# Kernel optimization log

Measured on AMD Instinct MI355X. Metric: run time of the kernel, lower is better.

The kernel has to match this reference:

```python
import jax, jax.numpy as jnp
import numpy as np

EMBED = 256
HEADS = 8
N_EDGES = 32  # topk k per query node = head_edges * heads = number_of_edges
HEAD_DIM = EMBED // HEADS


def setup_inputs() -> dict:
    key = jax.random.key(0)
    k1, k2, k3, k4 = jax.random.split(key, 4)
    B, L = 8, 2048
    return {
        "keys": jax.random.normal(k1, (B, L, EMBED), dtype=jnp.float32),
        "query": jax.random.normal(k2, (B, L, EMBED), dtype=jnp.float32),
        "Wk": jax.random.normal(k3, (HEAD_DIM, HEAD_DIM), dtype=jnp.float32) / np.sqrt(HEAD_DIM).astype(np.float32),
        "Wq": jax.random.normal(k4, (HEAD_DIM, HEAD_DIM), dtype=jnp.float32) / np.sqrt(HEAD_DIM).astype(np.float32),
    }


def reference(keys, query, Wk, Wq):
    B, Lk, _ = keys.shape
    Lq = query.shape[1]
    # split heads: [B, L, H, D]
    k = keys.reshape(B, Lk, HEADS, HEAD_DIM)
    q = query.reshape(B, Lq, HEADS, HEAD_DIM)
    # per-head linear projections (torch Linear: y = x @ W^T, no bias)
    k = jnp.einsum('nkhd,ed->nkhe', k, Wk)
    q = jnp.einsum('nqhd,ed->nqhe', q, Wq)
    # attention scores [B, H, Lq, Lk]
    energy = jnp.einsum('nqhd,nkhd->nhqk', q, k)
    attn = jax.nn.softmax(energy / jnp.sqrt(jnp.float32(EMBED)), axis=3)
    # mean over heads -> [B, Lq, Lk]
    mean_attn = jnp.mean(attn, axis=1)
    # topk neighbor indices per query node, then sorted ascending
    _, idx = jax.lax.top_k(mean_attn, N_EDGES)          # [B, Lq, N_EDGES]
    edges = jnp.sort(idx, axis=2)
    nodes = jnp.broadcast_to(jnp.arange(Lq, dtype=edges.dtype)[None, :, None], edges.shape)
    # edge_index [B, 2, Lq * N_EDGES]: row0 = source node, row1 = neighbor
    edge_index = jnp.stack([nodes.reshape(B, -1), edges.reshape(B, -1)], axis=1)
    return edge_index
```

## Files before the change

kernel.cpp:

```cpp
#include <hip/hip_runtime.h>
#include <hip/hip_bf16.h>

#define NB 8
#define LSEQ 2048
#define HH 8
#define DD 32
#define EE 256
#define NE 32
#define QT 16
#define NWAVE 16
#define NTH 1024
#define KW 128
#define NTILE 8
#define SMS 2050

typedef __attribute__((ext_vector_type(8))) short short8;
typedef __attribute__((ext_vector_type(4))) float f32x4;

__global__ __launch_bounds__(256) void proj_kernel(const float* __restrict__ x,
                                                   const float* __restrict__ W,
                                                   float scale,
                                                   __hip_bfloat16* __restrict__ o1,
                                                   __hip_bfloat16* __restrict__ o2,
                                                   __hip_bfloat16* __restrict__ o3) {
  const int b = blockIdx.x;
  __shared__ float xs[EE];
  __shared__ float Ws[DD][DD + 1];
  const int t = threadIdx.x;
  xs[t] = x[(size_t)b * EE + t];
  for (int i = t; i < DD * DD; i += 256) Ws[i / DD][i % DD] = W[i];
  __syncthreads();
  const int h = t / DD, e = t % DD;
  float acc = 0.f;
#pragma unroll
  for (int d = 0; d < DD; ++d) acc = fmaf(xs[h * DD + d], Ws[e][d], acc);
  acc *= scale;
  const int n = b / LSEQ, l = b % LSEQ;
  const size_t oi = (((size_t)n * HH + h) * LSEQ + l) * DD + e;
  __hip_bfloat16 p1 = __float2bfloat16(acc);
  float r1 = acc - __bfloat162float(p1);
  __hip_bfloat16 p2 = __float2bfloat16(r1);
  float r2 = r1 - __bfloat162float(p2);
  __hip_bfloat16 p3 = __float2bfloat16(r2);
  o1[oi] = p1;
  o2[oi] = p2;
  o3[oi] = p3;
}

__global__ __launch_bounds__(NTH) void attn_topk_kernel(
    const __hip_bfloat16* __restrict__ q1, const __hip_bfloat16* __restrict__ q2,
    const __hip_bfloat16* __restrict__ q3, const __hip_bfloat16* __restrict__ k1,
    const __hip_bfloat16* __restrict__ k2, const __hip_bfloat16* __restrict__ k3,
    int* __restrict__ out) {
  __shared__ float smean[QT * SMS];
  __shared__ float wredS[2][QT][NWAVE];

  const int t = threadIdx.x;
  const int w = t >> 6, l = t & 63;
  const int g = l >> 4, c = l & 15;
  const int n = blockIdx.x & 7;
  const int q0 = (blockIdx.x >> 3) * QT;

  for (int i = t; i < QT * SMS; i += NTH) smean[i] = 0.f;
  float* macc = &smean[(g * 4) * SMS + w * KW + c];
  __syncthreads();

  for (int h = 0; h < HH; ++h) {
    const size_t hb = ((size_t)n * HH + h) * LSEQ;
    const size_t qoff = (hb + q0 + c) * DD + (size_t)g * 8;
    const short8 aH = *(const short8*)(q1 + qoff);
    const short8 aM = *(const short8*)(q2 + qoff);
    const short8 aL = *(const short8*)(q3 + qoff);

    f32x4 acc[NTILE];
#pragma unroll
    for (int t2 = 0; t2 < NTILE; ++t2) {
      const size_t koff = (hb + (size_t)w * KW + t2 * 16 + c) * DD + (size_t)g * 8;
      const short8 bH = *(const short8*)(k1 + koff);
      const short8 bM = *(const short8*)(k2 + koff);
      const short8 bL = *(const short8*)(k3 + koff);
      f32x4 a = {0.f, 0.f, 0.f, 0.f};
      a = __builtin_amdgcn_mfma_f32_16x16x32_bf16(aH, bH, a, 0, 0, 0);
      a = __builtin_amdgcn_mfma_f32_16x16x32_bf16(aH, bM, a, 0, 0, 0);
      a = __builtin_amdgcn_mfma_f32_16x16x32_bf16(aM, bH, a, 0, 0, 0);
      a = __builtin_amdgcn_mfma_f32_16x16x32_bf16(aH, bL, a, 0, 0, 0);
      a = __builtin_amdgcn_mfma_f32_16x16x32_bf16(aL, bH, a, 0, 0, 0);
      a = __builtin_amdgcn_mfma_f32_16x16x32_bf16(aM, bM, a, 0, 0, 0);
      acc[t2] = a;
    }

    float Zl[4] = {0.f, 0.f, 0.f, 0.f};
#pragma unroll
    for (int t2 = 0; t2 < NTILE; ++t2) {
#pragma unroll
      for (int r = 0; r < 4; ++r) {
        float e = exp2f(acc[t2][r]);
        acc[t2][r] = e;
        Zl[r] += e;
      }
    }
#pragma unroll
    for (int msk = 1; msk <= 8; msk <<= 1)
#pragma unroll
      for (int r = 0; r < 4; ++r) Zl[r] += __shfl_xor(Zl[r], msk);
    if (c == 0) {
#pragma unroll
      for (int r = 0; r < 4; ++r) wredS[h & 1][g * 4 + r][w] = Zl[r];
    }
    __syncthreads();
    float inv[4];
#pragma unroll
    for (int r = 0; r < 4; ++r) {
      float z = wredS[h & 1][g * 4 + r][c];
#pragma unroll
      for (int msk = 1; msk <= 8; msk <<= 1) z += __shfl_xor(z, msk);
      inv[r] = __builtin_amdgcn_rcpf(z);
    }
#pragma unroll
    for (int t2 = 0; t2 < NTILE; ++t2)
#pragma unroll
      for (int r = 0; r < 4; ++r) {
        float* p = macc + r * SMS + t2 * 16;
        *p = fmaf(acc[t2][r], inv[r], *p);
      }
  }
  __syncthreads();

  float* row = &smean[w * SMS];
  float vals[32];
  float v1 = -1e30f, v2 = -1e30f;
  int i1 = 1 << 30, i2 = 1 << 30;
#pragma unroll
  for (int j = 0; j < 32; ++j) {
    float v = row[j * 64 + l];
    vals[j] = v;
    const int k = j * 64 + l;
    if (v > v1) { v2 = v1; i2 = i1; v1 = v; i1 = k; }
    else if (v > v2) { v2 = v; i2 = k; }
  }
  unsigned rem = 0u;
  int selk = 0;
#pragma unroll 1
  for (int it = 0; it < NE; ++it) {
    float bv = v1;
    int bk = i1;
#pragma unroll
    for (int off = 32; off >= 1; off >>= 1) {
      float ov = __shfl_xor(bv, off);
      int ok = __shfl_xor(bk, off);
      if (ov > bv || (ov == bv && ok < bk)) { bv = ov; bk = ok; }
    }
    if (l == it) selk = bk;
    if (i1 == bk) {
      rem |= 1u << (bk >> 6);
      if (i2 != (1 << 30)) {
        v1 = v2; i1 = i2;
        v2 = -1e30f; i2 = 1 << 30;
      } else {
        v1 = -1e30f; i1 = 1 << 30;
        v2 = -1e30f; i2 = 1 << 30;
#pragma unroll
        for (int j = 0; j < 32; ++j) {
          float v = ((rem >> j) & 1u) ? -1e30f : vals[j];
          const int k = j * 64 + l;
          if (v > v1) { v2 = v1; i2 = i1; v1 = v; i1 = k; }
          else if (v > v2) { v2 = v; i2 = k; }
        }
      }
    }
  }

  int rank = 0;
#pragma unroll
  for (int j = 0; j < NE; ++j) {
    int o = __shfl(selk, j);
    rank += (o < selk) ? 1 : 0;
  }
  const int qg = q0 + w;
  if (l < NE) {
    int* o0 = out + (size_t)n * 2 * LSEQ * NE + (size_t)qg * NE;
    int* o1p = o0 + (size_t)LSEQ * NE;
    o0[l] = qg;
    o1p[rank] = selk;
  }
}

extern "C" void kernel_launch(void* const* d_in, const int* in_sizes, int n_in,
                              void* d_out, int out_size, void* d_ws, size_t ws_size,
                              hipStream_t stream) {
  const float* keys = (const float*)d_in[0];
  const float* query = (const float*)d_in[1];
  const float* Wk = (const float*)d_in[2];
  const float* Wq = (const float*)d_in[3];
  int* out = (int*)d_out;

  const size_t SPLIT = (size_t)NB * HH * LSEQ * DD;
  __hip_bfloat16* qs1 = (__hip_bfloat16*)d_ws;
  __hip_bfloat16* qs2 = qs1 + SPLIT;
  __hip_bfloat16* qs3 = qs2 + SPLIT;
  __hip_bfloat16* ks1 = qs3 + SPLIT;
  __hip_bfloat16* ks2 = ks1 + SPLIT;
  __hip_bfloat16* ks3 = ks2 + SPLIT;

  proj_kernel<<<NB * LSEQ, 256, 0, stream>>>(query, Wq, 0.0625f * 1.44269504088896340736f,
                                             qs1, qs2, qs3);
  proj_kernel<<<NB * LSEQ, 256, 0, stream>>>(keys, Wk, 1.0f, ks1, ks2, ks3);
  attn_topk_kernel<<<NB * (LSEQ / QT), NTH, 0, stream>>>(qs1, qs2, qs3, ks1, ks2, ks3, out);
}
```

Before: 481.7 us.

## Precompute softmax normalizers in separate pass to remove per-head block barriers

```diff
diff --git a/kernel.cpp b/kernel.cpp
--- a/kernel.cpp
+++ b/kernel.cpp
@@ -8,11 +8,15 @@
 #define EE 256
 #define NE 32
 #define QT 16
-#define NWAVE 16
 #define NTH 1024
 #define KW 128
 #define NTILE 8
 #define SMS 2050
+
+#define ZQT 64
+#define ZNT 512
+#define ZKW 256
+#define ZNTILE 16
 
 typedef __attribute__((ext_vector_type(8))) short short8;
 typedef __attribute__((ext_vector_type(4))) float f32x4;
@@ -47,13 +51,81 @@
   o3[oi] = p3;
 }
 
+__global__ __launch_bounds__(ZNT) void zinv_kernel(
+    const __hip_bfloat16* __restrict__ q1, const __hip_bfloat16* __restrict__ q2,
+    const __hip_bfloat16* __restrict__ q3, const __hip_bfloat16* __restrict__ k1,
+    const __hip_bfloat16* __restrict__ k2, const __hip_bfloat16* __restrict__ k3,
+    float* __restrict__ invp) {
+  __shared__ float zlds[HH][ZQT];
+
+  const int t = threadIdx.x;
+  const int w = t >> 6, l = t & 63;
+  const int g = l >> 4, c = l & 15;
+  const int n = blockIdx.x & 7;
+  const int q0 = (blockIdx.x >> 3) * ZQT;
+
+  ((float*)zlds)[t] = 0.f;
+  __syncthreads();
+
+  for (int h = 0; h < HH; ++h) {
+    const size_t hb = ((size_t)n * HH + h) * LSEQ;
+    short8 aH[4], aM[4], aL[4];
+#pragma unroll
+    for (int qs = 0; qs < 4; ++qs) {
+      const size_t qoff = (hb + q0 + qs * 16 + c) * DD + (size_t)g * 8;
+      aH[qs] = *(const short8*)(q1 + qoff);
+      aM[qs] = *(const short8*)(q2 + qoff);
+      aL[qs] = *(const short8*)(q3 + qoff);
+    }
+    float Zl[4][4];
+#pragma unroll
+    for (int qs = 0; qs < 4; ++qs)
+#pragma unroll
+      for (int r = 0; r < 4; ++r) Zl[qs][r] = 0.f;
+
+    for (int t2 = 0; t2 < ZNTILE; ++t2) {
+      const size_t koff = (hb + (size_t)w * ZKW + t2 * 16 + c) * DD + (size_t)g * 8;
+      const short8 bH = *(const short8*)(k1 + koff);
+      const short8 bM = *(const short8*)(k2 + koff);
+      const short8 bL = *(const short8*)(k3 + koff);
+#pragma unroll
+      for (int qs = 0; qs < 4; ++qs) {
+        f32x4 a = {0.f, 0.f, 0.f, 0.f};
+        a = __builtin_amdgcn_mfma_f32_16x16x32_bf16(aH[qs], bH, a, 0, 0, 0);
+        a = __builtin_amdgcn_mfma_f32_16x16x32_bf16(aH[qs], bM, a, 0, 0, 0);
+        a = __builtin_amdgcn_mfma_f32_16x16x32_bf16(aM[qs], bH, a, 0, 0, 0);
+        a = __builtin_amdgcn_mfma_f32_16x16x32_bf16(aH[qs], bL, a, 0, 0, 0);
+        a = __builtin_amdgcn_mfma_f32_16x16x32_bf16(aL[qs], bH, a, 0, 0, 0);
+        a = __builtin_amdgcn_mfma_f32_16x16x32_bf16(aM[qs], bM, a, 0, 0, 0);
+#pragma unroll
+        for (int r = 0; r < 4; ++r) Zl[qs][r] += exp2f(a[r]);
+      }
+    }
+#pragma unroll
+    for (int msk = 1; msk <= 8; msk <<= 1)
+#pragma unroll
+      for (int qs = 0; qs < 4; ++qs)
+#pragma unroll
+        for (int r = 0; r < 4; ++r) Zl[qs][r] += __shfl_xor(Zl[qs][r], msk);
+    if (c == 0) {
+#pragma unroll
+      for (int qs = 0; qs < 4; ++qs)
+#pragma unroll
+        for (int r = 0; r < 4; ++r) atomicAdd(&zlds[h][qs * 16 + g * 4 + r], Zl[qs][r]);
+    }
+  }
+  __syncthreads();
+  const int h2 = t >> 6, qi = t & 63;
+  invp[((size_t)n * HH + h2) * LSEQ + q0 + qi] = __builtin_amdgcn_rcpf(zlds[h2][qi]);
+}
+
 __global__ __launch_bounds__(NTH) void attn_topk_kernel(
     const __hip_bfloat16* __restrict__ q1, const __hip_bfloat16* __restrict__ q2,
     const __hip_bfloat16* __restrict__ q3, const __hip_bfloat16* __restrict__ k1,
     const __hip_bfloat16* __restrict__ k2, const __hip_bfloat16* __restrict__ k3,
-    int* __restrict__ out) {
+    const float* __restrict__ invp, int* __restrict__ out) {
   __shared__ float smean[QT * SMS];
-  __shared__ float wredS[2][QT][NWAVE];
+  __shared__ float ilds[HH][QT];
 
   const int t = threadIdx.x;
   const int w = t >> 6, l = t & 63;
@@ -62,6 +134,10 @@
   const int q0 = (blockIdx.x >> 3) * QT;
 
   for (int i = t; i < QT * SMS; i += NTH) smean[i] = 0.f;
+  if (t < HH * QT) {
+    const int h = t >> 4, qi = t & 15;
+    ilds[h][qi] = invp[((size_t)n * HH + h) * LSEQ + q0 + qi];
+  }
   float* macc = &smean[(g * 4) * SMS + w * KW + c];
   __syncthreads();
 
@@ -71,8 +147,10 @@
     const short8 aH = *(const short8*)(q1 + qoff);
     const short8 aM = *(const short8*)(q2 + qoff);
     const short8 aL = *(const short8*)(q3 + qoff);
-
-    f32x4 acc[NTILE];
+    float iv[4];
+#pragma unroll
+    for (int r = 0; r < 4; ++r) iv[r] = ilds[h][g * 4 + r];
+
 #pragma unroll
     for (int t2 = 0; t2 < NTILE; ++t2) {
       const size_t koff = (hb + (size_t)w * KW + t2 * 16 + c) * DD + (size_t)g * 8;
@@ -86,43 +164,12 @@
       a = __builtin_amdgcn_mfma_f32_16x16x32_bf16(aH, bL, a, 0, 0, 0);
       a = __builtin_amdgcn_mfma_f32_16x16x32_bf16(aL, bH, a, 0, 0, 0);
       a = __builtin_amdgcn_mfma_f32_16x16x32_bf16(aM, bM, a, 0, 0, 0);
-      acc[t2] = a;
-    }
-
-    float Zl[4] = {0.f, 0.f, 0.f, 0.f};
-#pragma unroll
-    for (int t2 = 0; t2 < NTILE; ++t2) {
-#pragma unroll
-      for (int r = 0; r < 4; ++r) {
-        float e = exp2f(acc[t2][r]);
-        acc[t2][r] = e;
-        Zl[r] += e;
-      }
-    }
-#pragma unroll
-    for (int msk = 1; msk <= 8; msk <<= 1)
-#pragma unroll
-      for (int r = 0; r < 4; ++r) Zl[r] += __shfl_xor(Zl[r], msk);
-    if (c == 0) {
-#pragma unroll
-      for (int r = 0; r < 4; ++r) wredS[h & 1][g * 4 + r][w] = Zl[r];
-    }
-    __syncthreads();
-    float inv[4];
-#pragma unroll
-    for (int r = 0; r < 4; ++r) {
-      float z = wredS[h & 1][g * 4 + r][c];
-#pragma unroll
-      for (int msk = 1; msk <= 8; msk <<= 1) z += __shfl_xor(z, msk);
-      inv[r] = __builtin_amdgcn_rcpf(z);
-    }
-#pragma unroll
-    for (int t2 = 0; t2 < NTILE; ++t2)
 #pragma unroll
       for (int r = 0; r < 4; ++r) {
         float* p = macc + r * SMS + t2 * 16;
-        *p = fmaf(acc[t2][r], inv[r], *p);
+        *p = fmaf(exp2f(a[r]), iv[r], *p);
       }
+    }
   }
   __syncthreads();
 
@@ -201,9 +248,11 @@
   __hip_bfloat16* ks1 = qs3 + SPLIT;
   __hip_bfloat16* ks2 = ks1 + SPLIT;
   __hip_bfloat16* ks3 = ks2 + SPLIT;
+  float* invp = (float*)(ks3 + SPLIT);
 
   proj_kernel<<<NB * LSEQ, 256, 0, stream>>>(query, Wq, 0.0625f * 1.44269504088896340736f,
                                              qs1, qs2, qs3);
   proj_kernel<<<NB * LSEQ, 256, 0, stream>>>(keys, Wk, 1.0f, ks1, ks2, ks3);
-  attn_topk_kernel<<<NB * (LSEQ / QT), NTH, 0, stream>>>(qs1, qs2, qs3, ks1, ks2, ks3, out);
-}
+  zinv_kernel<<<NB * (LSEQ / ZQT), ZNT, 0, stream>>>(qs1, qs2, qs3, ks1, ks2, ks3, invp);
+  attn_topk_kernel<<<NB * (LSEQ / QT), NTH, 0, stream>>>(qs1, qs2, qs3, ks1, ks2, ks3, invp, out);
+}
```

New measurement: 526.0 us. 9.2% more time.
